# Kernel optimization log

Hardware: AMD Instinct MI355X
Metric: run time of the kernel (lower is better)

Reference implementation:

```python
import jax, jax.numpy as jnp
import numpy as np

B, I, H = 8192, 1024, 1024

def setup_inputs() -> dict:
    key = jax.random.key(0)
    ks = jax.random.split(key, 5)
    return {
        "x": jax.random.normal(ks[0], (B, I), dtype=jnp.float32),
        "m_prev": jax.random.normal(ks[1], (B, H), dtype=jnp.float32),
        "c_prev": jax.random.normal(ks[2], (B, H), dtype=jnp.float32),
        "w_m": jax.random.normal(ks[3], (H, 8 * H), dtype=jnp.float32),
        "w_inputs": jax.random.normal(ks[4], (I, 8 * H), dtype=jnp.float32),
    }

def reference(x, m_prev, c_prev, w_m, w_inputs):
    hidden = w_m.shape[0]
    m_mat = m_prev @ w_m              # [B, 8H]
    in_mat = x @ w_inputs             # [B, 8H]
    # 8-way split along feature dim
    ms = jnp.split(m_mat, 8, axis=1)
    xs = jnp.split(in_mat, 8, axis=1)
    sig, th, rl = jax.nn.sigmoid, jnp.tanh, jax.nn.relu
    l1_0 = sig(xs[0] + ms[0])
    l1_1 = rl(xs[1] + ms[1])
    l1_2 = sig(xs[2] + ms[2])
    l1_3 = rl(xs[3] * ms[3])
    l1_4 = th(xs[4] + ms[4])
    l1_5 = sig(xs[5] + ms[5])
    l1_6 = th(xs[6] + ms[6])
    l1_7 = sig(xs[7] + ms[7])
    l2_0 = th(l1_0 * l1_1)
    l2_1 = th(l1_2 + l1_3)
    l2_2 = th(l1_4 * l1_5)
    l2_3 = sig(l1_6 + l1_7)
    l2_0 = th(l2_0 + c_prev)
    new_c = l2_0 * l2_1
    l3_1 = th(l2_2 + l2_3)
    new_m = th(new_c * l3_1)
    return (new_m, new_c)
```

## Files before the change

kernel.cpp:

```cpp
#include <hip/hip_runtime.h>
#include <stdint.h>
#include <stddef.h>


typedef _Float16 half8 __attribute__((ext_vector_type(8)));
typedef float f32x4 __attribute__((ext_vector_type(4)));
typedef float float4v __attribute__((ext_vector_type(4)));
typedef unsigned int u32;
typedef u32 u32x4 __attribute__((ext_vector_type(4)));

__device__ __forceinline__ float fsig(float x) { return 1.0f / (1.0f + __expf(-x)); }
__device__ __forceinline__ float ftanh(float x) { return 2.0f * fsig(2.0f * x) - 1.0f; }
__device__ __forceinline__ u32 packh(_Float16 a, _Float16 b) {
  union { u32 u; _Float16 h[2]; } p;
  p.h[0] = a; p.h[1] = b; return p.u;
}

__device__ __forceinline__ void gload16(const void* g, void* l) {
  __builtin_amdgcn_global_load_lds(
      (const __attribute__((address_space(1))) void*)g,
      (__attribute__((address_space(3))) void*)l, 16, 0, 0);
}

__global__ __launch_bounds__(256) void prep_b(
    const float* __restrict__ w_inputs, const float* __restrict__ w_m,
    u32* __restrict__ wsB) {
  const int kt = blockIdx.x;
  const int hblk = blockIdx.y;
  const int tid = threadIdx.x;
  const int n = tid & 15;
  const int g = (tid >> 4) & 7;
  const int mat = tid >> 7;
  const float* w = mat ? w_m : w_inputs;
  const float* src = w + (size_t)kt * 32 * 8192 + (size_t)g * 1024 + hblk * 16 + n;
  const int kx4 = ((n >> 1) & 3) << 2;
  u32 hw[16], lw[16];
#pragma unroll
  for (int k2 = 0; k2 < 16; ++k2) {
    const float v0 = src[(size_t)(2 * k2) * 8192];
    const float v1 = src[(size_t)(2 * k2 + 1) * 8192];
    const _Float16 h0 = (_Float16)v0, h1 = (_Float16)v1;
    hw[k2 ^ kx4] = packh(h0, h1);
    lw[k2 ^ kx4] = packh((_Float16)(v0 - (float)h0), (_Float16)(v1 - (float)h1));
  }
  u32* dhi = wsB + ((size_t)kt * 64 + hblk) * 8192 + mat * 2048 + g * 256 + n * 16;
  u32* dlo = dhi + 4096;
#pragma unroll
  for (int t4 = 0; t4 < 4; ++t4) {
    u32x4 a = {hw[t4 * 4], hw[t4 * 4 + 1], hw[t4 * 4 + 2], hw[t4 * 4 + 3]};
    *(u32x4*)(dhi + t4 * 4) = a;
    u32x4 b = {lw[t4 * 4], lw[t4 * 4 + 1], lw[t4 * 4 + 2], lw[t4 * 4 + 3]};
    *(u32x4*)(dlo + t4 * 4) = b;
  }
}

__global__ __launch_bounds__(256) void split_a(
    const float4v* __restrict__ in, half8* __restrict__ hi, half8* __restrict__ lo) {
  const size_t idx = (size_t)blockIdx.x * 256 + threadIdx.x;
  const float4v a = in[idx * 2];
  const float4v b = in[idx * 2 + 1];
  half8 h, l;
#pragma unroll
  for (int j = 0; j < 4; ++j) {
    const float v = a[j]; const _Float16 hv = (_Float16)v;
    h[j] = hv; l[j] = (_Float16)(v - (float)hv);
  }
#pragma unroll
  for (int j = 0; j < 4; ++j) {
    const float v = b[j]; const _Float16 hv = (_Float16)v;
    h[4 + j] = hv; l[4 + j] = (_Float16)(v - (float)hv);
  }
  hi[idx] = h; lo[idx] = l;
}

__global__ __launch_bounds__(256, 2) void nascell_fast(
    const _Float16* __restrict__ xh_g, const _Float16* __restrict__ xl_g,
    const _Float16* __restrict__ mh_g, const _Float16* __restrict__ ml_g,
    const u32* __restrict__ wsB,
    const float* __restrict__ c_prev,
    float* __restrict__ out) {
  __shared__ short lds[32768];
  const int tid = threadIdx.x;
  const int wid = tid >> 6;
  const int lane = tid & 63;
  const int row0 = blockIdx.y * 256;
  const int hblk = blockIdx.x;
  const int m16 = lane & 15;
  const int q = lane >> 4;
  const int qsw = (q ^ ((m16 >> 1) & 3)) * 8;

  const size_t arow = (size_t)(row0 + wid * 64 + m16);
  const _Float16* xhb = xh_g + arow * 1024 + q * 8;
  const _Float16* xlb = xl_g + arow * 1024 + q * 8;
  const _Float16* mhb = mh_g + arow * 1024 + q * 8;
  const _Float16* mlb = ml_g + arow * 1024 + q * 8;

  const char* wsb = (const char*)wsB + (size_t)hblk * 32768 + wid * 8192 + lane * 16;
  char* ldsb0 = (char*)lds + wid * 8192;

  f32x4 acc[4][9];
#pragma unroll
  for (int r = 0; r < 4; ++r)
#pragma unroll
    for (int gg = 0; gg < 9; ++gg) acc[r][gg] = (f32x4)0.0f;

#pragma unroll
  for (int i = 0; i < 8; ++i) gload16(wsb + i * 1024, ldsb0 + i * 1024);

  for (int kt = 0; kt < 32; ++kt) {
    __syncthreads();

    half8 axh[4], axl[4], amh[4], aml[4];
#pragma unroll
    for (int r = 0; r < 4; ++r) {
      axh[r] = *(const half8*)(xhb + (size_t)r * 16384 + kt * 32);
      axl[r] = *(const half8*)(xlb + (size_t)r * 16384 + kt * 32);
      amh[r] = *(const half8*)(mhb + (size_t)r * 16384 + kt * 32);
      aml[r] = *(const half8*)(mlb + (size_t)r * 16384 + kt * 32);
    }
    __builtin_amdgcn_sched_barrier(0);
    if (kt < 31) {
      const char* src = wsb + (size_t)(kt + 1) * 2097152;
      char* dst = (char*)lds + ((kt + 1) & 1) * 32768 + wid * 8192;
#pragma unroll
      for (int i = 0; i < 8; ++i) gload16(src + i * 1024, dst + i * 1024);
    }
    __builtin_amdgcn_sched_barrier(0);

    const short* bb = lds + (kt & 1) * 16384;

#pragma unroll
    for (int c = 0; c < 8; ++c) {
      const int bo = c * 512 + m16 * 32 + qsw;
      const half8 bxh = *(const half8*)(bb + bo);
      const half8 bxl = *(const half8*)(bb + 8192 + bo);
#pragma unroll
      for (int r = 0; r < 4; ++r) {
        f32x4 t = acc[r][c];
        t = __builtin_amdgcn_mfma_f32_16x16x32_f16(axh[r], bxh, t, 0, 0, 0);
        t = __builtin_amdgcn_mfma_f32_16x16x32_f16(axh[r], bxl, t, 0, 0, 0);
        t = __builtin_amdgcn_mfma_f32_16x16x32_f16(axl[r], bxh, t, 0, 0, 0);
        acc[r][c] = t;
      }
    }

#pragma unroll
    for (int c = 0; c < 8; ++c) {
      const int bo = 4096 + c * 512 + m16 * 32 + qsw;
      const half8 bmh = *(const half8*)(bb + bo);
      const half8 bml = *(const half8*)(bb + 8192 + bo);
      const int tgt = (c == 3) ? 8 : c;
#pragma unroll
      for (int r = 0; r < 4; ++r) {
        f32x4 t = acc[r][tgt];
        t = __builtin_amdgcn_mfma_f32_16x16x32_f16(amh[r], bmh, t, 0, 0, 0);
        t = __builtin_amdgcn_mfma_f32_16x16x32_f16(amh[r], bml, t, 0, 0, 0);
        t = __builtin_amdgcn_mfma_f32_16x16x32_f16(aml[r], bmh, t, 0, 0, 0);
        acc[r][tgt] = t;
      }
    }
  }

  float* out_m = out;
  float* out_c = out + (size_t)8192 * 1024;
  const int h = hblk * 16 + m16;
#pragma unroll
  for (int r = 0; r < 4; ++r) {
#pragma unroll
    for (int i = 0; i < 4; ++i) {
      const int grow = row0 + wid * 64 + r * 16 + q * 4 + i;
      const float p0 = acc[r][0][i], p1 = acc[r][1][i], p2 = acc[r][2][i];
      const float x3 = acc[r][3][i], p4 = acc[r][4][i], p5 = acc[r][5][i];
      const float p6 = acc[r][6][i], p7 = acc[r][7][i], m3 = acc[r][8][i];
      const float cp = c_prev[(size_t)grow * 1024 + h];
      float l1_0 = fsig(p0);
      float l1_1 = fmaxf(p1, 0.0f);
      float l1_2 = fsig(p2);
      float l1_3 = fmaxf(x3 * m3, 0.0f);
      float l1_4 = ftanh(p4);
      float l1_5 = fsig(p5);
      float l1_6 = ftanh(p6);
      float l1_7 = fsig(p7);
      float l2_0 = ftanh(l1_0 * l1_1);
      float l2_1 = ftanh(l1_2 + l1_3);
      float l2_2 = ftanh(l1_4 * l1_5);
      float l2_3 = fsig(l1_6 + l1_7);
      float l2_0b = ftanh(l2_0 + cp);
      float nc = l2_0b * l2_1;
      float l3_1 = ftanh(l2_2 + l2_3);
      float nm = ftanh(nc * l3_1);
      out_m[(size_t)grow * 1024 + h] = nm;
      out_c[(size_t)grow * 1024 + h] = nc;
    }
  }
}

__global__ __launch_bounds__(256, 2) void nascell_main(
    const float* __restrict__ x,
    const float* __restrict__ m_prev,
    const float* __restrict__ c_prev,
    const float* __restrict__ w_inputs,
    const float* __restrict__ w_m,
    float* __restrict__ out) {
  __shared__ short lds[17408];
  const int tid = threadIdx.x;
  const int wid = tid >> 6;
  const int lane = tid & 63;
  const int row0 = blockIdx.y * 256;
  const int h0 = blockIdx.x * 16;
  const int m16 = lane & 15;
  const int q = lane >> 4;

  const int bmat = tid >> 7;
  const int bg = (tid >> 4) & 7;
  const int bkp = (tid & 15) * 2;
  const float* wsrc = bmat ? w_m : w_inputs;
  const float* wrow_base = wsrc + (size_t)bkp * 8192 + (size_t)bg * 1024 + (size_t)h0;
  short* bh = lds + bmat * 4352 + bg * 544 + (bkp ^ ((bg & 3) << 3));
  short* bl = bh + 8704;

  const float* axp[4];
  const float* amp[4];
#pragma unroll
  for (int r = 0; r < 4; ++r) {
    const size_t arow = (size_t)(row0 + wid * 64 + r * 16 + m16);
    axp[r] = x + arow * 1024 + q * 8;
    amp[r] = m_prev + arow * 1024 + q * 8;
  }

  f32x4 acc[4][9];
#pragma unroll
  for (int r = 0; r < 4; ++r)
#pragma unroll
    for (int gg = 0; gg < 9; ++gg) acc[r][gg] = (f32x4)0.0f;

  for (int kt = 0; kt < 32; ++kt) {
    const float* wr = wrow_base + (size_t)kt * 32 * 8192;
    float4v b0 = *(const float4v*)(wr);
    float4v b1 = *(const float4v*)(wr + 4);
    float4v b2 = *(const float4v*)(wr + 8);
    float4v b3 = *(const float4v*)(wr + 12);
    float4v d0 = *(const float4v*)(wr + 8192);
    float4v d1 = *(const float4v*)(wr + 8196);
    float4v d2 = *(const float4v*)(wr + 8200);
    float4v d3 = *(const float4v*)(wr + 8204);

    float4v xa[4][2];
#pragma unroll
    for (int r = 0; r < 4; ++r) {
      xa[r][0] = *(const float4v*)(axp[r] + kt * 32);
      xa[r][1] = *(const float4v*)(axp[r] + kt * 32 + 4);
    }

    __syncthreads();

#pragma unroll
    for (int n = 0; n < 16; ++n) {
      const float r0 = (n < 4 ? b0[n & 3] : n < 8 ? b1[n & 3] : n < 12 ? b2[n & 3] : b3[n & 3]);
      const float r1 = (n < 4 ? d0[n & 3] : n < 8 ? d1[n & 3] : n < 12 ? d2[n & 3] : d3[n & 3]);
      const _Float16 h0v = (_Float16)r0;
      const _Float16 h1v = (_Float16)r1;
      *(u32*)(bh + n * 32) = packh(h0v, h1v);
      const _Float16 l0v = (_Float16)(r0 - (float)h0v);
      const _Float16 l1v = (_Float16)(r1 - (float)h1v);
      *(u32*)(bl + n * 32) = packh(l0v, l1v);
    }

    half8 axh[4], axl[4];
#pragma unroll
    for (int r = 0; r < 4; ++r)
#pragma unroll
      for (int j = 0; j < 8; ++j) {
        const float v = xa[r][j >> 2][j & 3];
        const _Float16 hv = (_Float16)v;
        axh[r][j] = hv;
        axl[r][j] = (_Float16)(v - (float)hv);
      }

    __syncthreads();

    float4v ma[4][2];
#pragma unroll
    for (int r = 0; r < 4; ++r) {
      ma[r][0] = *(const float4v*)(amp[r] + kt * 32);
      ma[r][1] = *(const float4v*)(amp[r] + kt * 32 + 4);
    }

#pragma unroll
    for (int c = 0; c < 8; ++c) {
      const int qs = (q ^ (c & 3)) * 8;
      const int bo = c * 544 + m16 * 32 + qs;
      half8 bxh = *(const half8*)(lds + bo);
      half8 bxl = *(const half8*)(lds + 8704 + bo);
#pragma unroll
      for (int r = 0; r < 4; ++r) {
        f32x4 t = acc[r][c];
        t = __builtin_amdgcn_mfma_f32_16x16x32_f16(axh[r], bxh, t, 0, 0, 0);
        t = __builtin_amdgcn_mfma_f32_16x16x32_f16(axh[r], bxl, t, 0, 0, 0);
        t = __builtin_amdgcn_mfma_f32_16x16x32_f16(axl[r], bxh, t, 0, 0, 0);
        acc[r][c] = t;
      }
    }

    half8 amh[4], aml[4];
#pragma unroll
    for (int r = 0; r < 4; ++r)
#pragma unroll
      for (int j = 0; j < 8; ++j) {
        const float v = ma[r][j >> 2][j & 3];
        const _Float16 hv = (_Float16)v;
        amh[r][j] = hv;
        aml[r][j] = (_Float16)(v - (float)hv);
      }

#pragma unroll
    for (int c = 0; c < 8; ++c) {
      const int qs = (q ^ (c & 3)) * 8;
      const int bo = 4352 + c * 544 + m16 * 32 + qs;
      half8 bmh = *(const half8*)(lds + bo);
      half8 bml = *(const half8*)(lds + 8704 + bo);
      const int tgt = (c == 3) ? 8 : c;
#pragma unroll
      for (int r = 0; r < 4; ++r) {
        f32x4 t = acc[r][tgt];
        t = __builtin_amdgcn_mfma_f32_16x16x32_f16(amh[r], bmh, t, 0, 0, 0);
        t = __builtin_amdgcn_mfma_f32_16x16x32_f16(amh[r], bml, t, 0, 0, 0);
        t = __builtin_amdgcn_mfma_f32_16x16x32_f16(aml[r], bmh, t, 0, 0, 0);
        acc[r][tgt] = t;
      }
    }
  }

  float* out_m = out;
  float* out_c = out + (size_t)8192 * 1024;
  const int h = h0 + m16;
#pragma unroll
  for (int r = 0; r < 4; ++r) {
#pragma unroll
    for (int i = 0; i < 4; ++i) {
      const int grow = row0 + wid * 64 + r * 16 + q * 4 + i;
      const float p0 = acc[r][0][i], p1 = acc[r][1][i], p2 = acc[r][2][i];
      const float x3 = acc[r][3][i], p4 = acc[r][4][i], p5 = acc[r][5][i];
      const float p6 = acc[r][6][i], p7 = acc[r][7][i], m3 = acc[r][8][i];
      const float cp = c_prev[(size_t)grow * 1024 + h];
      float l1_0 = fsig(p0);
      float l1_1 = fmaxf(p1, 0.0f);
      float l1_2 = fsig(p2);
      float l1_3 = fmaxf(x3 * m3, 0.0f);
      float l1_4 = ftanh(p4);
      float l1_5 = fsig(p5);
      float l1_6 = ftanh(p6);
      float l1_7 = fsig(p7);
      float l2_0 = ftanh(l1_0 * l1_1);
      float l2_1 = ftanh(l1_2 + l1_3);
      float l2_2 = ftanh(l1_4 * l1_5);
      float l2_3 = fsig(l1_6 + l1_7);
      float l2_0b = ftanh(l2_0 + cp);
      float nc = l2_0b * l2_1;
      float l3_1 = ftanh(l2_2 + l2_3);
      float nm = ftanh(nc * l3_1);
      out_m[(size_t)grow * 1024 + h] = nm;
      out_c[(size_t)grow * 1024 + h] = nc;
    }
  }
}

extern "C" void kernel_launch(void* const* d_in, const int* in_sizes, int n_in,
                              void* d_out, int out_size, void* d_ws, size_t ws_size,
                              hipStream_t stream) {
  (void)in_sizes; (void)n_in; (void)out_size;
  const float* x        = (const float*)d_in[0];
  const float* m_prev   = (const float*)d_in[1];
  const float* c_prev   = (const float*)d_in[2];
  const float* w_m      = (const float*)d_in[3];
  const float* w_inputs = (const float*)d_in[4];
  float* out = (float*)d_out;

  if (ws_size >= 134217728ull && d_ws != nullptr) {
    u32* wsB = (u32*)d_ws;
    _Float16* xh = (_Float16*)((char*)d_ws + 67108864);
    _Float16* xl = xh + 8388608;
    _Float16* mh = xl + 8388608;
    _Float16* ml = mh + 8388608;
    prep_b<<<dim3(32, 64), 256, 0, stream>>>(w_inputs, w_m, wsB);
    split_a<<<4096, 256, 0, stream>>>((const float4v*)x, (half8*)xh, (half8*)xl);
    split_a<<<4096, 256, 0, stream>>>((const float4v*)m_prev, (half8*)mh, (half8*)ml);
    nascell_fast<<<dim3(64, 32), 256, 0, stream>>>(xh, xl, mh, ml, wsB, c_prev, out);
  } else {
    dim3 grid(64, 32);
    nascell_main<<<grid, 256, 0, stream>>>(x, m_prev, c_prev, w_inputs, w_m, out);
  }
}
```

Measured before the change: 873.0 us.

## Merge prep kernels and widen GEMM block to 512 threads sharing A tiles

```diff
diff --git a/kernel.cpp b/kernel.cpp
--- a/kernel.cpp
+++ b/kernel.cpp
@@ -22,81 +22,245 @@
       (__attribute__((address_space(3))) void*)l, 16, 0, 0);
 }
 
-__global__ __launch_bounds__(256) void prep_b(
+__global__ __launch_bounds__(256) void prep_all(
     const float* __restrict__ w_inputs, const float* __restrict__ w_m,
-    u32* __restrict__ wsB) {
-  const int kt = blockIdx.x;
-  const int hblk = blockIdx.y;
+    const float4v* __restrict__ xin, const float4v* __restrict__ min,
+    u32* __restrict__ wsB,
+    half8* __restrict__ xhi, half8* __restrict__ xlo,
+    half8* __restrict__ mhi, half8* __restrict__ mlo) {
+  const int bid = blockIdx.x;
   const int tid = threadIdx.x;
-  const int n = tid & 15;
-  const int g = (tid >> 4) & 7;
-  const int mat = tid >> 7;
-  const float* w = mat ? w_m : w_inputs;
-  const float* src = w + (size_t)kt * 32 * 8192 + (size_t)g * 1024 + hblk * 16 + n;
-  const int kx4 = ((n >> 1) & 3) << 2;
-  u32 hw[16], lw[16];
-#pragma unroll
-  for (int k2 = 0; k2 < 16; ++k2) {
-    const float v0 = src[(size_t)(2 * k2) * 8192];
-    const float v1 = src[(size_t)(2 * k2 + 1) * 8192];
-    const _Float16 h0 = (_Float16)v0, h1 = (_Float16)v1;
-    hw[k2 ^ kx4] = packh(h0, h1);
-    lw[k2 ^ kx4] = packh((_Float16)(v0 - (float)h0), (_Float16)(v1 - (float)h1));
-  }
-  u32* dhi = wsB + ((size_t)kt * 64 + hblk) * 8192 + mat * 2048 + g * 256 + n * 16;
-  u32* dlo = dhi + 4096;
-#pragma unroll
-  for (int t4 = 0; t4 < 4; ++t4) {
-    u32x4 a = {hw[t4 * 4], hw[t4 * 4 + 1], hw[t4 * 4 + 2], hw[t4 * 4 + 3]};
-    *(u32x4*)(dhi + t4 * 4) = a;
-    u32x4 b = {lw[t4 * 4], lw[t4 * 4 + 1], lw[t4 * 4 + 2], lw[t4 * 4 + 3]};
-    *(u32x4*)(dlo + t4 * 4) = b;
-  }
-}
-
-__global__ __launch_bounds__(256) void split_a(
-    const float4v* __restrict__ in, half8* __restrict__ hi, half8* __restrict__ lo) {
-  const size_t idx = (size_t)blockIdx.x * 256 + threadIdx.x;
-  const float4v a = in[idx * 2];
-  const float4v b = in[idx * 2 + 1];
-  half8 h, l;
-#pragma unroll
-  for (int j = 0; j < 4; ++j) {
-    const float v = a[j]; const _Float16 hv = (_Float16)v;
-    h[j] = hv; l[j] = (_Float16)(v - (float)hv);
-  }
-#pragma unroll
-  for (int j = 0; j < 4; ++j) {
-    const float v = b[j]; const _Float16 hv = (_Float16)v;
-    h[4 + j] = hv; l[4 + j] = (_Float16)(v - (float)hv);
-  }
-  hi[idx] = h; lo[idx] = l;
-}
-
-__global__ __launch_bounds__(256, 2) void nascell_fast(
+  if (bid < 2048) {
+    const int kt = bid & 31;
+    const int hblk = bid >> 5;
+    const int n = tid & 15;
+    const int g = (tid >> 4) & 7;
+    const int mat = tid >> 7;
+    const float* w = mat ? w_m : w_inputs;
+    const float* src = w + (size_t)kt * 32 * 8192 + (size_t)g * 1024 + hblk * 16 + n;
+    const int kx4 = ((n >> 1) & 3) << 2;
+    u32 hw[16], lw[16];
+#pragma unroll
+    for (int k2 = 0; k2 < 16; ++k2) {
+      const float v0 = src[(size_t)(2 * k2) * 8192];
+      const float v1 = src[(size_t)(2 * k2 + 1) * 8192];
+      const _Float16 h0 = (_Float16)v0, h1 = (_Float16)v1;
+      hw[k2 ^ kx4] = packh(h0, h1);
+      lw[k2 ^ kx4] = packh((_Float16)(v0 - (float)h0), (_Float16)(v1 - (float)h1));
+    }
+    u32* dhi = wsB + ((size_t)(hblk * 32 + kt) * 2 + mat) * 4096 + g * 256 + n * 16;
+    u32* dlo = dhi + 2048;
+#pragma unroll
+    for (int t4 = 0; t4 < 4; ++t4) {
+      u32x4 a = {hw[t4 * 4], hw[t4 * 4 + 1], hw[t4 * 4 + 2], hw[t4 * 4 + 3]};
+      *(u32x4*)(dhi + t4 * 4) = a;
+      u32x4 b = {lw[t4 * 4], lw[t4 * 4 + 1], lw[t4 * 4 + 2], lw[t4 * 4 + 3]};
+      *(u32x4*)(dlo + t4 * 4) = b;
+    }
+  } else {
+    const int sid = bid - 2048;
+    const int which = sid >> 12;
+    const int bx = sid & 4095;
+    const float4v* in = which ? min : xin;
+    half8* hi = which ? mhi : xhi;
+    half8* lo = which ? mlo : xlo;
+    const size_t idx = (size_t)bx * 256 + tid;
+    const float4v a = in[idx * 2];
+    const float4v b = in[idx * 2 + 1];
+    half8 h, l;
+#pragma unroll
+    for (int j = 0; j < 4; ++j) {
+      const float v = a[j]; const _Float16 hv = (_Float16)v;
+      h[j] = hv; l[j] = (_Float16)(v - (float)hv);
+    }
+#pragma unroll
+    for (int j = 0; j < 4; ++j) {
+      const float v = b[j]; const _Float16 hv = (_Float16)v;
+      h[4 + j] = hv; l[4 + j] = (_Float16)(v - (float)hv);
+    }
+    hi[idx] = h; lo[idx] = l;
+  }
+}
+
+
+#define NAS_STG(KT, MAT, BUFB)                                              \
+  do {                                                                      \
+    const char* s_ = (const char*)wsB +                                     \
+        (((size_t)(2 * hb2 + cgs) * 32 + (size_t)(KT)) * 2 + (MAT)) * 16384 \
+        + tg * 16;                                                          \
+    char* d_ = ldsc + (BUFB) + cgs * 16384 + tg * 16;                       \
+    gload16(s_, d_);                                                        \
+    gload16(s_ + 4096, d_ + 4096);                                          \
+    gload16(s_ + 8192, d_ + 8192);                                          \
+    gload16(s_ + 12288, d_ + 12288);                                        \
+  } while (0)
+
+#define NAS_LOADX(KT)                                                       \
+  do {                                                                      \
+    _Pragma("unroll") for (int r_ = 0; r_ < 4; ++r_) {                      \
+      axh[r_] = *(const half8*)(xhb + r_ * 16384 + (KT) * 32);              \
+      axl[r_] = *(const half8*)(xlb + r_ * 16384 + (KT) * 32);              \
+    }                                                                       \
+  } while (0)
+
+#define NAS_LOADM(KT)                                                       \
+  do {                                                                      \
+    _Pragma("unroll") for (int r_ = 0; r_ < 4; ++r_) {                      \
+      amh[r_] = *(const half8*)(mhb + r_ * 16384 + (KT) * 32);              \
+      aml[r_] = *(const half8*)(mlb + r_ * 16384 + (KT) * 32);              \
+    }                                                                       \
+  } while (0)
+
+__global__ __launch_bounds__(512, 2) void nascell_v7(
     const _Float16* __restrict__ xh_g, const _Float16* __restrict__ xl_g,
     const _Float16* __restrict__ mh_g, const _Float16* __restrict__ ml_g,
     const u32* __restrict__ wsB,
     const float* __restrict__ c_prev,
     float* __restrict__ out) {
-  __shared__ short lds[32768];
+  __shared__ short lds_s[32768];
+  char* ldsc = (char*)lds_s;
+  const int tid = threadIdx.x;
+  const int wid = tid >> 6;
+  const int lane = tid & 63;
+  const int wr = wid >> 1;
+  const int cg = wid & 1;
+  const int row0 = blockIdx.y * 256;
+  const int hb2 = blockIdx.x;
+  const int m16 = lane & 15;
+  const int q = lane >> 4;
+  const int qsw = (q ^ ((m16 >> 1) & 3)) * 8;
+
+  const int tg = tid & 255;
+  const int cgs = tid >> 8;
+
+  const _Float16* xhb = xh_g + (size_t)(row0 + wr * 64 + m16) * 1024 + q * 8;
+  const _Float16* xlb = xl_g + (size_t)(row0 + wr * 64 + m16) * 1024 + q * 8;
+  const _Float16* mhb = mh_g + (size_t)(row0 + wr * 64 + m16) * 1024 + q * 8;
+  const _Float16* mlb = ml_g + (size_t)(row0 + wr * 64 + m16) * 1024 + q * 8;
+
+  f32x4 acc[4][9];
+#pragma unroll
+  for (int r = 0; r < 4; ++r)
+#pragma unroll
+    for (int gg = 0; gg < 9; ++gg) acc[r][gg] = (f32x4)0.0f;
+
+  half8 axh[4], axl[4], amh[4], aml[4];
+
+  const short* bbx = lds_s + cg * 8192;
+  const short* bbm = lds_s + 16384 + cg * 8192;
+
+  NAS_STG(0, 0, 0);
+  NAS_LOADX(0);
+
+#pragma unroll 1
+  for (int kt = 0; kt < 32; ++kt) {
+    __syncthreads();
+    NAS_STG(kt, 1, 32768);
+    NAS_LOADM(kt);
+    __builtin_amdgcn_sched_barrier(0);
+#pragma unroll
+    for (int c = 0; c < 8; ++c) {
+      const int bo = c * 512 + m16 * 32 + qsw;
+      const half8 bh = *(const half8*)(bbx + bo);
+      const half8 bl = *(const half8*)(bbx + 4096 + bo);
+#pragma unroll
+      for (int r = 0; r < 4; ++r) {
+        f32x4 t = acc[r][c];
+        t = __builtin_amdgcn_mfma_f32_16x16x32_f16(axh[r], bh, t, 0, 0, 0);
+        t = __builtin_amdgcn_mfma_f32_16x16x32_f16(axh[r], bl, t, 0, 0, 0);
+        t = __builtin_amdgcn_mfma_f32_16x16x32_f16(axl[r], bh, t, 0, 0, 0);
+        acc[r][c] = t;
+      }
+    }
+    __syncthreads();
+    if (kt < 31) {
+      NAS_STG(kt + 1, 0, 0);
+      NAS_LOADX(kt + 1);
+    }
+    __builtin_amdgcn_sched_barrier(0);
+#pragma unroll
+    for (int c = 0; c < 8; ++c) {
+      const int bo = c * 512 + m16 * 32 + qsw;
+      const half8 bh = *(const half8*)(bbm + bo);
+      const half8 bl = *(const half8*)(bbm + 4096 + bo);
+      const int tgt = (c == 3) ? 8 : c;
+#pragma unroll
+      for (int r = 0; r < 4; ++r) {
+        f32x4 t = acc[r][tgt];
+        t = __builtin_amdgcn_mfma_f32_16x16x32_f16(amh[r], bh, t, 0, 0, 0);
+        t = __builtin_amdgcn_mfma_f32_16x16x32_f16(amh[r], bl, t, 0, 0, 0);
+        t = __builtin_amdgcn_mfma_f32_16x16x32_f16(aml[r], bh, t, 0, 0, 0);
+        acc[r][tgt] = t;
+      }
+    }
+  }
+
+  float* out_m = out;
+  float* out_c = out + (size_t)8192 * 1024;
+  const int h = hb2 * 32 + cg * 16 + m16;
+#pragma unroll
+  for (int r = 0; r < 4; ++r) {
+#pragma unroll
+    for (int i = 0; i < 4; ++i) {
+      const int grow = row0 + wr * 64 + r * 16 + q * 4 + i;
+      const float p0 = acc[r][0][i], p1 = acc[r][1][i], p2 = acc[r][2][i];
+      const float x3 = acc[r][3][i], p4 = acc[r][4][i], p5 = acc[r][5][i];
+      const float p6 = acc[r][6][i], p7 = acc[r][7][i], m3 = acc[r][8][i];
+      const float cp = c_prev[(size_t)grow * 1024 + h];
+      float l1_0 = fsig(p0);
+      float l1_1 = fmaxf(p1, 0.0f);
+      float l1_2 = fsig(p2);
+      float l1_3 = fmaxf(x3 * m3, 0.0f);
+      float l1_4 = ftanh(p4);
+      float l1_5 = fsig(p5);
+      float l1_6 = ftanh(p6);
+      float l1_7 = fsig(p7);
+      float l2_0 = ftanh(l1_0 * l1_1);
+      float l2_1 = ftanh(l1_2 + l1_3);
+      float l2_2 = ftanh(l1_4 * l1_5);
+      float l2_3 = fsig(l1_6 + l1_7);
+      float l2_0b = ftanh(l2_0 + cp);
+      float nc = l2_0b * l2_1;
+      float l3_1 = ftanh(l2_2 + l2_3);
+      float nm = ftanh(nc * l3_1);
+      out_m[(size_t)grow * 1024 + h] = nm;
+      out_c[(size_t)grow * 1024 + h] = nc;
+    }
+  }
+}
+
+__global__ __launch_bounds__(256, 2) void nascell_main(
+    const float* __restrict__ x,
+    const float* __restrict__ m_prev,
+    const float* __restrict__ c_prev,
+    const float* __restrict__ w_inputs,
+    const float* __restrict__ w_m,
+    float* __restrict__ out) {
+  __shared__ short lds[17408];
   const int tid = threadIdx.x;
   const int wid = tid >> 6;
   const int lane = tid & 63;
   const int row0 = blockIdx.y * 256;
-  const int hblk = blockIdx.x;
+  const int h0 = blockIdx.x * 16;
   const int m16 = lane & 15;
   const int q = lane >> 4;
-  const int qsw = (q ^ ((m16 >> 1) & 3)) * 8;
-
-  const size_t arow = (size_t)(row0 + wid * 64 + m16);
-  const _Float16* xhb = xh_g + arow * 1024 + q * 8;
-  const _Float16* xlb = xl_g + arow * 1024 + q * 8;
-  const _Float16* mhb = mh_g + arow * 1024 + q * 8;
-  const _Float16* mlb = ml_g + arow * 1024 + q * 8;
-
-  const char* wsb = (const char*)wsB + (size_t)hblk * 32768 + wid * 8192 + lane * 16;
-  char* ldsb0 = (char*)lds + wid * 8192;
+
+  const int bmat = tid >> 7;
+  const int bg = (tid >> 4) & 7;
+  const int bkp = (tid & 15) * 2;
+  const float* wsrc = bmat ? w_m : w_inputs;
+  const float* wrow_base = wsrc + (size_t)bkp * 8192 + (size_t)bg * 1024 + (size_t)h0;
+  short* bh = lds + bmat * 4352 + bg * 544 + (bkp ^ ((bg & 3) << 3));
+  short* bl = bh + 8704;
+
+  const float* axp[4];
+  const float* amp[4];
+#pragma unroll
+  for (int r = 0; r < 4; ++r) {
+    const size_t arow = (size_t)(row0 + wid * 64 + r * 16 + m16);
+    axp[r] = x + arow * 1024 + q * 8;
+    amp[r] = m_prev + arow * 1024 + q * 8;
+  }
 
   f32x4 acc[4][9];
 #pragma unroll
@@ -104,36 +268,64 @@
 #pragma unroll
     for (int gg = 0; gg < 9; ++gg) acc[r][gg] = (f32x4)0.0f;
 
-#pragma unroll
-  for (int i = 0; i < 8; ++i) gload16(wsb + i * 1024, ldsb0 + i * 1024);
-
   for (int kt = 0; kt < 32; ++kt) {
+    const float* wr = wrow_base + (size_t)kt * 32 * 8192;
+    float4v b0 = *(const float4v*)(wr);
+    float4v b1 = *(const float4v*)(wr + 4);
+    float4v b2 = *(const float4v*)(wr + 8);
+    float4v b3 = *(const float4v*)(wr + 12);
+    float4v d0 = *(const float4v*)(wr + 8192);
+    float4v d1 = *(const float4v*)(wr + 8196);
+    float4v d2 = *(const float4v*)(wr + 8200);
+    float4v d3 = *(const float4v*)(wr + 8204);
+
+    float4v xa[4][2];
+#pragma unroll
+    for (int r = 0; r < 4; ++r) {
+      xa[r][0] = *(const float4v*)(axp[r] + kt * 32);
+      xa[r][1] = *(const float4v*)(axp[r] + kt * 32 + 4);
+    }
+
     __syncthreads();
 
-    half8 axh[4], axl[4], amh[4], aml[4];
+#pragma unroll
+    for (int n = 0; n < 16; ++n) {
+      const float r0 = (n < 4 ? b0[n & 3] : n < 8 ? b1[n & 3] : n < 12 ? b2[n & 3] : b3[n & 3]);
+      const float r1 = (n < 4 ? d0[n & 3] : n < 8 ? d1[n & 3] : n < 12 ? d2[n & 3] : d3[n & 3]);
+      const _Float16 h0v = (_Float16)r0;
+      const _Float16 h1v = (_Float16)r1;
+      *(u32*)(bh + n * 32) = packh(h0v, h1v);
+      const _Float16 l0v = (_Float16)(r0 - (float)h0v);
+      const _Float16 l1v = (_Float16)(r1 - (float)h1v);
+      *(u32*)(bl + n * 32) = packh(l0v, l1v);
+    }
+
+    half8 axh[4], axl[4];
+#pragma unroll
+    for (int r = 0; r < 4; ++r)
+#pragma unroll
+      for (int j = 0; j < 8; ++j) {
+        const float v = xa[r][j >> 2][j & 3];
+        const _Float16 hv = (_Float16)v;
+        axh[r][j] = hv;
+        axl[r][j] = (_Float16)(v - (float)hv);
+      }
+
+    __syncthreads();
+
+    float4v ma[4][2];
 #pragma unroll
     for (int r = 0; r < 4; ++r) {
-      axh[r] = *(const half8*)(xhb + (size_t)r * 16384 + kt * 32);
-      axl[r] = *(const half8*)(xlb + (size_t)r * 16384 + kt * 32);
-      amh[r] = *(const half8*)(mhb + (size_t)r * 16384 + kt * 32);
-      aml[r] = *(const half8*)(mlb + (size_t)r * 16384 + kt * 32);
-    }
-    __builtin_amdgcn_sched_barrier(0);
-    if (kt < 31) {
-      const char* src = wsb + (size_t)(kt + 1) * 2097152;
-      char* dst = (char*)lds + ((kt + 1) & 1) * 32768 + wid * 8192;
-#pragma unroll
-      for (int i = 0; i < 8; ++i) gload16(src + i * 1024, dst + i * 1024);
-    }
-    __builtin_amdgcn_sched_barrier(0);
-
-    const short* bb = lds + (kt & 1) * 16384;
+      ma[r][0] = *(const float4v*)(amp[r] + kt * 32);
+      ma[r][1] = *(const float4v*)(amp[r] + kt * 32 + 4);
+    }
 
 #pragma unroll
     for (int c = 0; c < 8; ++c) {
-      const int bo = c * 512 + m16 * 32 + qsw;
-      const half8 bxh = *(const half8*)(bb + bo);
-      const half8 bxl = *(const half8*)(bb + 8192 + bo);
+      const int qs = (q ^ (c & 3)) * 8;
+      const int bo = c * 544 + m16 * 32 + qs;
+      half8 bxh = *(const half8*)(lds + bo);
+      half8 bxl = *(const half8*)(lds + 8704 + bo);
 #pragma unroll
       for (int r = 0; r < 4; ++r) {
         f32x4 t = acc[r][c];
@@ -144,11 +336,23 @@
       }
     }
 
+    half8 amh[4], aml[4];
+#pragma unroll
+    for (int r = 0; r < 4; ++r)
+#pragma unroll
+      for (int j = 0; j < 8; ++j) {
+        const float v = ma[r][j >> 2][j & 3];
+        const _Float16 hv = (_Float16)v;
+        amh[r][j] = hv;
+        aml[r][j] = (_Float16)(v - (float)hv);
+      }
+
 #pragma unroll
     for (int c = 0; c < 8; ++c) {
-      const int bo = 4096 + c * 512 + m16 * 32 + qsw;
-      const half8 bmh = *(const half8*)(bb + bo);
-      const half8 bml = *(const half8*)(bb + 8192 + bo);
+      const int qs = (q ^ (c & 3)) * 8;
+      const int bo = 4352 + c * 544 + m16 * 32 + qs;
+      half8 bmh = *(const half8*)(lds + bo);
+      half8 bml = *(const half8*)(lds + 8704 + bo);
       const int tgt = (c == 3) ? 8 : c;
 #pragma unroll
       for (int r = 0; r < 4; ++r) {
@@ -163,7 +367,7 @@
 
   float* out_m = out;
   float* out_c = out + (size_t)8192 * 1024;
-  const int h = hblk * 16 + m16;
+  const int h = h0 + m16;
 #pragma unroll
   for (int r = 0; r < 4; ++r) {
 #pragma unroll
@@ -195,176 +399,6 @@
   }
 }
 
-__global__ __launch_bounds__(256, 2) void nascell_main(
-    const float* __restrict__ x,
-    const float* __restrict__ m_prev,
-    const float* __restrict__ c_prev,
-    const float* __restrict__ w_inputs,
-    const float* __restrict__ w_m,
-    float* __restrict__ out) {
-  __shared__ short lds[17408];
-  const int tid = threadIdx.x;
-  const int wid = tid >> 6;
-  const int lane = tid & 63;
-  const int row0 = blockIdx.y * 256;
-  const int h0 = blockIdx.x * 16;
-  const int m16 = lane & 15;
-  const int q = lane >> 4;
-
-  const int bmat = tid >> 7;
-  const int bg = (tid >> 4) & 7;
-  const int bkp = (tid & 15) * 2;
-  const float* wsrc = bmat ? w_m : w_inputs;
-  const float* wrow_base = wsrc + (size_t)bkp * 8192 + (size_t)bg * 1024 + (size_t)h0;
-  short* bh = lds + bmat * 4352 + bg * 544 + (bkp ^ ((bg & 3) << 3));
-  short* bl = bh + 8704;
-
-  const float* axp[4];
-  const float* amp[4];
-#pragma unroll
-  for (int r = 0; r < 4; ++r) {
-    const size_t arow = (size_t)(row0 + wid * 64 + r * 16 + m16);
-    axp[r] = x + arow * 1024 + q * 8;
-    amp[r] = m_prev + arow * 1024 + q * 8;
-  }
-
-  f32x4 acc[4][9];
-#pragma unroll
-  for (int r = 0; r < 4; ++r)
-#pragma unroll
-    for (int gg = 0; gg < 9; ++gg) acc[r][gg] = (f32x4)0.0f;
-
-  for (int kt = 0; kt < 32; ++kt) {
-    const float* wr = wrow_base + (size_t)kt * 32 * 8192;
-    float4v b0 = *(const float4v*)(wr);
-    float4v b1 = *(const float4v*)(wr + 4);
-    float4v b2 = *(const float4v*)(wr + 8);
-    float4v b3 = *(const float4v*)(wr + 12);
-    float4v d0 = *(const float4v*)(wr + 8192);
-    float4v d1 = *(const float4v*)(wr + 8196);
-    float4v d2 = *(const float4v*)(wr + 8200);
-    float4v d3 = *(const float4v*)(wr + 8204);
-
-    float4v xa[4][2];
-#pragma unroll
-    for (int r = 0; r < 4; ++r) {
-      xa[r][0] = *(const float4v*)(axp[r] + kt * 32);
-      xa[r][1] = *(const float4v*)(axp[r] + kt * 32 + 4);
-    }
-
-    __syncthreads();
-
-#pragma unroll
-    for (int n = 0; n < 16; ++n) {
-      const float r0 = (n < 4 ? b0[n & 3] : n < 8 ? b1[n & 3] : n < 12 ? b2[n & 3] : b3[n & 3]);
-      const float r1 = (n < 4 ? d0[n & 3] : n < 8 ? d1[n & 3] : n < 12 ? d2[n & 3] : d3[n & 3]);
-      const _Float16 h0v = (_Float16)r0;
-      const _Float16 h1v = (_Float16)r1;
-      *(u32*)(bh + n * 32) = packh(h0v, h1v);
-      const _Float16 l0v = (_Float16)(r0 - (float)h0v);
-      const _Float16 l1v = (_Float16)(r1 - (float)h1v);
-      *(u32*)(bl + n * 32) = packh(l0v, l1v);
-    }
-
-    half8 axh[4], axl[4];
-#pragma unroll
-    for (int r = 0; r < 4; ++r)
-#pragma unroll
-      for (int j = 0; j < 8; ++j) {
-        const float v = xa[r][j >> 2][j & 3];
-        const _Float16 hv = (_Float16)v;
-        axh[r][j] = hv;
-        axl[r][j] = (_Float16)(v - (float)hv);
-      }
-
-    __syncthreads();
-
-    float4v ma[4][2];
-#pragma unroll
-    for (int r = 0; r < 4; ++r) {
-      ma[r][0] = *(const float4v*)(amp[r] + kt * 32);
-      ma[r][1] = *(const float4v*)(amp[r] + kt * 32 + 4);
-    }
-
-#pragma unroll
-    for (int c = 0; c < 8; ++c) {
-      const int qs = (q ^ (c & 3)) * 8;
-      const int bo = c * 544 + m16 * 32 + qs;
-      half8 bxh = *(const half8*)(lds + bo);
-      half8 bxl = *(const half8*)(lds + 8704 + bo);
-#pragma unroll
-      for (int r = 0; r < 4; ++r) {
-        f32x4 t = acc[r][c];
-        t = __builtin_amdgcn_mfma_f32_16x16x32_f16(axh[r], bxh, t, 0, 0, 0);
-        t = __builtin_amdgcn_mfma_f32_16x16x32_f16(axh[r], bxl, t, 0, 0, 0);
-        t = __builtin_amdgcn_mfma_f32_16x16x32_f16(axl[r], bxh, t, 0, 0, 0);
-        acc[r][c] = t;
-      }
-    }
-
-    half8 amh[4], aml[4];
-#pragma unroll
-    for (int r = 0; r < 4; ++r)
-#pragma unroll
-      for (int j = 0; j < 8; ++j) {
-        const float v = ma[r][j >> 2][j & 3];
-        const _Float16 hv = (_Float16)v;
-        amh[r][j] = hv;
-        aml[r][j] = (_Float16)(v - (float)hv);
-      }
-
-#pragma unroll
-    for (int c = 0; c < 8; ++c) {
-      const int qs = (q ^ (c & 3)) * 8;
-      const int bo = 4352 + c * 544 + m16 * 32 + qs;
-      half8 bmh = *(const half8*)(lds + bo);
-      half8 bml = *(const half8*)(lds + 8704 + bo);
-      const int tgt = (c == 3) ? 8 : c;
-#pragma unroll
-      for (int r = 0; r < 4; ++r) {
-        f32x4 t = acc[r][tgt];
-        t = __builtin_amdgcn_mfma_f32_16x16x32_f16(amh[r], bmh, t, 0, 0, 0);
-        t = __builtin_amdgcn_mfma_f32_16x16x32_f16(amh[r], bml, t, 0, 0, 0);
-        t = __builtin_amdgcn_mfma_f32_16x16x32_f16(aml[r], bmh, t, 0, 0, 0);
-        acc[r][tgt] = t;
-      }
-    }
-  }
-
-  float* out_m = out;
-  float* out_c = out + (size_t)8192 * 1024;
-  const int h = h0 + m16;
-#pragma unroll
-  for (int r = 0; r < 4; ++r) {
-#pragma unroll
-    for (int i = 0; i < 4; ++i) {
-      const int grow = row0 + wid * 64 + r * 16 + q * 4 + i;
-      const float p0 = acc[r][0][i], p1 = acc[r][1][i], p2 = acc[r][2][i];
-      const float x3 = acc[r][3][i], p4 = acc[r][4][i], p5 = acc[r][5][i];
-      const float p6 = acc[r][6][i], p7 = acc[r][7][i], m3 = acc[r][8][i];
-      const float cp = c_prev[(size_t)grow * 1024 + h];
-      float l1_0 = fsig(p0);
-      float l1_1 = fmaxf(p1, 0.0f);
-      float l1_2 = fsig(p2);
-      float l1_3 = fmaxf(x3 * m3, 0.0f);
-      float l1_4 = ftanh(p4);
-      float l1_5 = fsig(p5);
-      float l1_6 = ftanh(p6);
-      float l1_7 = fsig(p7);
-      float l2_0 = ftanh(l1_0 * l1_1);
-      float l2_1 = ftanh(l1_2 + l1_3);
-      float l2_2 = ftanh(l1_4 * l1_5);
-      float l2_3 = fsig(l1_6 + l1_7);
-      float l2_0b = ftanh(l2_0 + cp);
-      float nc = l2_0b * l2_1;
-      float l3_1 = ftanh(l2_2 + l2_3);
-      float nm = ftanh(nc * l3_1);
-      out_m[(size_t)grow * 1024 + h] = nm;
-      out_c[(size_t)grow * 1024 + h] = nc;
-    }
-  }
-}
-
 extern "C" void kernel_launch(void* const* d_in, const int* in_sizes, int n_in,
                               void* d_out, int out_size, void* d_ws, size_t ws_size,
                               hipStream_t stream) {
@@ -382,10 +416,11 @@
     _Float16* xl = xh + 8388608;
     _Float16* mh = xl + 8388608;
     _Float16* ml = mh + 8388608;
-    prep_b<<<dim3(32, 64), 256, 0, stream>>>(w_inputs, w_m, wsB);
-    split_a<<<4096, 256, 0, stream>>>((const float4v*)x, (half8*)xh, (half8*)xl);
-    split_a<<<4096, 256, 0, stream>>>((const float4v*)m_prev, (half8*)mh, (half8*)ml);
-    nascell_fast<<<dim3(64, 32), 256, 0, stream>>>(xh, xl, mh, ml, wsB, c_prev, out);
+    prep_all<<<10240, 256, 0, stream>>>(
+        w_inputs, w_m, (const float4v*)x, (const float4v*)m_prev, wsB,
+        (half8*)xh, (half8*)xl, (half8*)mh, (half8*)ml);
+    nascell_v7<<<dim3(32, 32), 512, 0, stream>>>(
+        xh, xl, mh, ml, wsB, c_prev, out);
   } else {
     dim3 grid(64, 32);
     nascell_main<<<grid, 256, 0, stream>>>(x, m_prev, c_prev, w_inputs, w_m, out);
```

Result: slower. 1.035 ms (+18.6%).
